# Optimization experiments

Hardware: AMD Instinct MI355X
Metric: run time of the kernel (lower is better)

## Reference

```python
import jax, jax.numpy as jnp
import numpy as np

B, S, H = 2, 4096, 1024  # batch, seq_len, hidden_size (= all_head_size)


def setup_inputs() -> dict:
    key = jax.random.key(0)
    ks = jax.random.split(key, 7)
    sc = 1.0 / np.sqrt(H)
    return {
        "hidden_states": jax.random.normal(ks[0], (B, S, H), dtype=jnp.float32),
        "Wq": jax.random.normal(ks[1], (H, H), dtype=jnp.float32) * sc,
        "bq": jnp.zeros((H,), dtype=jnp.float32),
        "Wk": jax.random.normal(ks[2], (H, H), dtype=jnp.float32) * sc,
        "bk": jnp.zeros((H,), dtype=jnp.float32),
        "Wv": jax.random.normal(ks[3], (H, H), dtype=jnp.float32) * sc,
        "bv": jnp.zeros((H,), dtype=jnp.float32),
    }


def reference(hidden_states, Wq, bq, Wk, bk, Wv, bv):
    # QKV projections (weights stored as [in, out] = W.T of torch Linear)
    q = hidden_states @ Wq + bq  # [B,S,H]
    k = hidden_states @ Wk + bk
    v = hidden_states @ Wv + bv
    # Raw attention: no head split, no 1/sqrt(d) scaling (faithful to source)
    scores = jnp.einsum("bqh,bkh->bqk", q, k)  # [B,S,S]
    probs = jax.nn.softmax(scores, axis=-1)
    context = jnp.einsum("bqk,bkh->bqh", probs, v)  # [B,S,H]
    return context
```

## Files before the change

kernel.cpp:

```cpp
#include <hip/hip_runtime.h>
#include <stdint.h>

typedef __attribute__((ext_vector_type(8))) short short8;
typedef __attribute__((ext_vector_type(8))) _Float16 half8;
typedef __attribute__((ext_vector_type(4))) float f32x4;

__device__ __forceinline__ unsigned short f2h(float x) {
  _Float16 h = (_Float16)x;
  return __builtin_bit_cast(unsigned short, h);
}
__device__ __forceinline__ float h2f(unsigned short u) {
  return (float)__builtin_bit_cast(_Float16, u);
}

#define GLOAD16(gsrc, ldst)                                              \
  __builtin_amdgcn_global_load_lds(                                      \
      (const __attribute__((address_space(1))) void*)(gsrc),             \
      (__attribute__((address_space(3))) void*)(ldst), 16, 0, 0)

#define VM(N) asm volatile("s_waitcnt vmcnt(" #N ")" ::: "memory")
#define BARSYNC __builtin_amdgcn_s_barrier()

__global__ __launch_bounds__(256) void split_pair_f16_kernel(
    const float* __restrict__ in, unsigned short* __restrict__ h,
    unsigned short* __restrict__ l) {
  size_t i = (size_t)blockIdx.x * 256 + threadIdx.x;
  float4 v = ((const float4*)in)[i];
  unsigned short h0 = f2h(v.x), h1 = f2h(v.y), h2 = f2h(v.z), h3 = f2h(v.w);
  ((ushort4*)h)[i] = make_ushort4(h0, h1, h2, h3);
  ((ushort4*)l)[i] = make_ushort4(f2h(v.x - h2f(h0)), f2h(v.y - h2f(h1)),
                                  f2h(v.z - h2f(h2)), f2h(v.w - h2f(h3)));
}

__global__ __launch_bounds__(256) void transpose_f16_kernel(
    const float* __restrict__ W, unsigned short* __restrict__ hT,
    int Kd, int Nd) {
  __shared__ float tile[32][33];
  int r = threadIdx.x >> 3;
  int c = (threadIdx.x & 7) * 4;
  int k0 = blockIdx.y * 32, n0 = blockIdx.x * 32;
  float4 v = *(const float4*)&W[(size_t)(k0 + r) * Nd + n0 + c];
  tile[r][c] = v.x; tile[r][c + 1] = v.y; tile[r][c + 2] = v.z; tile[r][c + 3] = v.w;
  __syncthreads();
  size_t o = (size_t)(n0 + r) * Kd + k0 + c;
  *(ushort4*)&hT[o] = make_ushort4(f2h(tile[c + 0][r]), f2h(tile[c + 1][r]),
                                   f2h(tile[c + 2][r]), f2h(tile[c + 3][r]));
}

template <int OM>
__global__ __launch_bounds__(512, 2) void g2_kernel(
    const unsigned short* __restrict__ Ah, const unsigned short* __restrict__ Al,
    const unsigned short* __restrict__ Bh, const float* __restrict__ bias,
    unsigned short* __restrict__ out0, int K, int lda, int ldb, int ldo) {
  __shared__ __align__(16) char smem[3 * 40 * 1024];

  const int t = threadIdx.x;
  const int wid = t >> 6, lane = t & 63;
  const int waveM = wid >> 2, waveN = wid & 3;
  const int lr0 = lane & 15, lk0 = (lane >> 4) * 8;
  const int m0 = blockIdx.y * 256, n0 = blockIdx.x * 128;

  const unsigned short* slot_src[5];
#pragma unroll
  for (int s = 0; s < 5; ++s) {
    int si = 5 * wid + s;
    const unsigned short* base;
    size_t roff;
    if (si < 16)      { base = Ah; roff = (size_t)(m0 + si * 16 + lr0) * lda; }
    else if (si < 32) { base = Al; roff = (size_t)(m0 + (si - 16) * 16 + lr0) * lda; }
    else              { base = Bh; roff = (size_t)(n0 + (si - 32) * 16 + lr0) * ldb; }
    slot_src[s] = base + roff + lk0;
  }

  const int NTILES = K >> 5;
  f32x4 acc[8][2] = {};

#pragma unroll
  for (int tt = 0; tt < 2; ++tt)
#pragma unroll
    for (int s = 0; s < 5; ++s)
      GLOAD16(slot_src[s] + (size_t)tt * 32,
              smem + tt * 40960 + (5 * wid + s) * 1024);
  VM(5);
  BARSYNC;
  __builtin_amdgcn_sched_barrier(0);

  for (int tile = 0; tile < NTILES; ++tile) {
    const int cur = tile % 3;
    const int nxt = (tile + 2) % 3;
    const bool do_stage = (tile + 2) < NTILES;
    const char* cb = smem + cur * 40960;
    char* nb = smem + nxt * 40960;
    half8 bf[2];
#pragma unroll
    for (int p = 0; p < 4; ++p) {
      half8 ahf[2], alf[2];
#pragma unroll
      for (int i = 0; i < 2; ++i) {
        int mg = waveM * 8 + 2 * p + i;
        ahf[i] = *(const half8*)(cb + mg * 1024 + lane * 16);
        alf[i] = *(const half8*)(cb + (16 + mg) * 1024 + lane * 16);
      }
      if (p == 0) {
#pragma unroll
        for (int j = 0; j < 2; ++j) {
          int ng = waveN * 2 + j;
          bf[j] = *(const half8*)(cb + (32 + ng) * 1024 + lane * 16);
        }
      }
      if (do_stage) {
        if (p == 0) {
          GLOAD16(slot_src[0] + (size_t)(tile + 2) * 32, nb + (5 * wid + 0) * 1024);
          GLOAD16(slot_src[1] + (size_t)(tile + 2) * 32, nb + (5 * wid + 1) * 1024);
        } else {
          const int slot = p + 1;
          GLOAD16(slot_src[slot] + (size_t)(tile + 2) * 32,
                  nb + (5 * wid + slot) * 1024);
        }
      }
      __builtin_amdgcn_s_setprio(1);
#pragma unroll
      for (int i = 0; i < 2; ++i)
#pragma unroll
        for (int j = 0; j < 2; ++j) {
          f32x4 c = acc[2 * p + i][j];
          c = __builtin_amdgcn_mfma_f32_16x16x32_f16(ahf[i], bf[j], c, 0, 0, 0);
          c = __builtin_amdgcn_mfma_f32_16x16x32_f16(alf[i], bf[j], c, 0, 0, 0);
          acc[2 * p + i][j] = c;
        }
      __builtin_amdgcn_s_setprio(0);
      if (p < 3) __builtin_amdgcn_s_barrier();
    }
    if (tile + 1 < NTILES) {
      if (do_stage) VM(5); else VM(0);
      BARSYNC;
      __builtin_amdgcn_sched_barrier(0);
    }
  }

  const int or0 = (lane >> 4) * 4;
#pragma unroll
  for (int mm = 0; mm < 8; ++mm)
#pragma unroll
    for (int j = 0; j < 2; ++j)
#pragma unroll
      for (int r = 0; r < 4; ++r) {
        int row = m0 + waveM * 128 + mm * 16 + or0 + r;
        int col = n0 + waveN * 32 + j * 16 + lr0;
        float x = acc[mm][j][r] + bias[col];
        if constexpr (OM == 4) {
          out0[(size_t)row * ldo + col] = f2h(x);
        } else {
          out0[(size_t)col * ldo + row] = f2h(x);
        }
      }
}

__global__ __launch_bounds__(512, 2) void g1_kernel(
    const unsigned short* __restrict__ Abase, size_t Astr, int lda,
    const unsigned short* __restrict__ Bbase, size_t Bstr, int ldb,
    float* __restrict__ outF, size_t Ostr, int ldo, int K) {
  __shared__ __align__(16) char smem[3 * 48 * 1024];
  const int t = threadIdx.x, wid = t >> 6, lane = t & 63;
  const int waveM = wid >> 2, waveN = wid & 3;
  const int lr0 = lane & 15, lk0 = (lane >> 4) * 8;
  const int m0 = blockIdx.y * 256, n0 = blockIdx.x * 128;
  const unsigned short* A = Abase + (size_t)blockIdx.z * Astr;
  const unsigned short* B = Bbase + (size_t)blockIdx.z * Bstr;
  float* out = outF + (size_t)blockIdx.z * Ostr;

  const unsigned short* slot_src[6];
#pragma unroll
  for (int s = 0; s < 6; ++s) {
    int si = 6 * wid + s;
    const unsigned short* p;
    if (si < 16)      p = A + (size_t)(m0 + si * 16 + lr0) * lda + lk0;
    else if (si < 32) p = A + (size_t)(m0 + (si - 16) * 16 + lr0) * lda + 32 + lk0;
    else if (si < 40) p = B + (size_t)(n0 + (si - 32) * 16 + lr0) * ldb + lk0;
    else              p = B + (size_t)(n0 + (si - 40) * 16 + lr0) * ldb + 32 + lk0;
    slot_src[s] = p;
  }

  const int NTILES = K >> 6;
  f32x4 acc[8][2] = {};

#pragma unroll
  for (int tt = 0; tt < 2; ++tt)
#pragma unroll
    for (int s = 0; s < 6; ++s)
      GLOAD16(slot_src[s] + (size_t)tt * 64,
              smem + tt * 49152 + (6 * wid + s) * 1024);
  VM(6);
  BARSYNC;
  __builtin_amdgcn_sched_barrier(0);

  for (int tile = 0; tile < NTILES; ++tile) {
    const int cur = tile % 3, nxt = (tile + 2) % 3;
    const bool do_stage = (tile + 2) < NTILES;
    const char* cb = smem + cur * 49152;
    char* nb = smem + nxt * 49152;
    half8 blo[2], bhi[2];
#pragma unroll
    for (int p = 0; p < 4; ++p) {
      half8 alo[2], ahi[2];
#pragma unroll
      for (int i = 0; i < 2; ++i) {
        int mg = waveM * 8 + 2 * p + i;
        alo[i] = *(const half8*)(cb + mg * 1024 + lane * 16);
        ahi[i] = *(const half8*)(cb + (16 + mg) * 1024 + lane * 16);
      }
      if (p == 0) {
#pragma unroll
        for (int j = 0; j < 2; ++j) {
          int ng = waveN * 2 + j;
          blo[j] = *(const half8*)(cb + (32 + ng) * 1024 + lane * 16);
          bhi[j] = *(const half8*)(cb + (40 + ng) * 1024 + lane * 16);
        }
      }
      if (do_stage && p < 3) {
#pragma unroll
        for (int s = 0; s < 2; ++s) {
          int slot = 2 * p + s;
          GLOAD16(slot_src[slot] + (size_t)(tile + 2) * 64,
                  nb + (6 * wid + slot) * 1024);
        }
      }
      __builtin_amdgcn_s_setprio(1);
#pragma unroll
      for (int i = 0; i < 2; ++i)
#pragma unroll
        for (int j = 0; j < 2; ++j) {
          f32x4 c = acc[2 * p + i][j];
          c = __builtin_amdgcn_mfma_f32_16x16x32_f16(alo[i], blo[j], c, 0, 0, 0);
          c = __builtin_amdgcn_mfma_f32_16x16x32_f16(ahi[i], bhi[j], c, 0, 0, 0);
          acc[2 * p + i][j] = c;
        }
      __builtin_amdgcn_s_setprio(0);
      if (p < 3) __builtin_amdgcn_s_barrier();
    }
    if (tile + 1 < NTILES) {
      if (do_stage) VM(6); else VM(0);
      BARSYNC;
      __builtin_amdgcn_sched_barrier(0);
    }
  }

  const int or0 = (lane >> 4) * 4;
#pragma unroll
  for (int mm = 0; mm < 8; ++mm)
#pragma unroll
    for (int j = 0; j < 2; ++j)
#pragma unroll
      for (int r = 0; r < 4; ++r)
        out[(size_t)(m0 + waveM * 128 + mm * 16 + or0 + r) * ldo +
            (n0 + waveN * 32 + j * 16 + lr0)] = acc[mm][j][r];
}

__global__ __launch_bounds__(256) void softmax_rows_kernel(
    const float* Sm, unsigned short* P, int ncol, int pld) {
  const int t = threadIdx.x;
  const float* srow = Sm + (size_t)blockIdx.x * ncol;
  float4 v[4];
  float m = -3.4e38f;
#pragma unroll
  for (int i = 0; i < 4; ++i) {
    v[i] = ((const float4*)srow)[t + 256 * i];
    m = fmaxf(m, fmaxf(fmaxf(v[i].x, v[i].y), fmaxf(v[i].z, v[i].w)));
  }
#pragma unroll
  for (int off = 32; off >= 1; off >>= 1) m = fmaxf(m, __shfl_down(m, off));
  __shared__ float redm[4];
  if ((t & 63) == 0) redm[t >> 6] = m;
  __syncthreads();
  m = fmaxf(fmaxf(redm[0], redm[1]), fmaxf(redm[2], redm[3]));
  float s = 0.f;
#pragma unroll
  for (int i = 0; i < 4; ++i) {
    v[i].x = __expf(v[i].x - m);
    v[i].y = __expf(v[i].y - m);
    v[i].z = __expf(v[i].z - m);
    v[i].w = __expf(v[i].w - m);
    s += v[i].x + v[i].y + v[i].z + v[i].w;
  }
#pragma unroll
  for (int off = 32; off >= 1; off >>= 1) s += __shfl_down(s, off);
  __shared__ float reds[4];
  if ((t & 63) == 0) reds[t >> 6] = s;
  __syncthreads();
  s = reds[0] + reds[1] + reds[2] + reds[3];
  float inv = 1.f / s;
  unsigned short* prow = P + (size_t)blockIdx.x * pld;
#pragma unroll
  for (int i = 0; i < 4; ++i) {
    ushort4 o = make_ushort4(f2h(v[i].x * inv), f2h(v[i].y * inv),
                             f2h(v[i].z * inv), f2h(v[i].w * inv));
    ((ushort4*)prow)[t + 256 * i] = o;
  }
}

extern "C" void kernel_launch(void* const* d_in, const int* in_sizes, int n_in,
                              void* d_out, int out_size, void* d_ws, size_t ws_size,
                              hipStream_t stream) {
  const float* hs = (const float*)d_in[0];
  const float* Wq = (const float*)d_in[1];
  const float* bq = (const float*)d_in[2];
  const float* Wk = (const float*)d_in[3];
  const float* bk = (const float*)d_in[4];
  const float* Wv = (const float*)d_in[5];
  const float* bv = (const float*)d_in[6];
  float* out = (float*)d_out;

  constexpr int Ss = 4096, Hh = 1024;
  constexpr int Mm = 8192;
  constexpr size_t TOK = (size_t)Ss * Hh;
  char* ws = (char*)d_ws;
  const size_t MB = 1024 * 1024;

  unsigned short* qh = (unsigned short*)(ws + 0 * MB);
  unsigned short* kh = (unsigned short*)(ws + 16 * MB);
  unsigned short* vT = (unsigned short*)(ws + 32 * MB);
  char* rb = ws + 48 * MB;
  unsigned short* hs_h = (unsigned short*)(rb + 0 * MB);
  unsigned short* hs_l = (unsigned short*)(rb + 16 * MB);
  unsigned short* Wqh = (unsigned short*)(rb + 32 * MB);
  unsigned short* Wkh = (unsigned short*)(rb + 34 * MB);
  unsigned short* Wvh = (unsigned short*)(rb + 36 * MB);
  float* Sf = (float*)rb;

  const bool big = ws_size >= (size_t)176 * MB;

  split_pair_f16_kernel<<<dim3(Mm * Hh / 1024), 256, 0, stream>>>(hs, hs_h, hs_l);
  transpose_f16_kernel<<<dim3(32, 32), 256, 0, stream>>>(Wq, Wqh, Hh, Hh);
  transpose_f16_kernel<<<dim3(32, 32), 256, 0, stream>>>(Wk, Wkh, Hh, Hh);
  transpose_f16_kernel<<<dim3(32, 32), 256, 0, stream>>>(Wv, Wvh, Hh, Hh);

  g2_kernel<4><<<dim3(8, 32), 512, 0, stream>>>(hs_h, hs_l, Wqh, bq, qh, Hh, Hh, Hh, Hh);
  g2_kernel<4><<<dim3(8, 32), 512, 0, stream>>>(hs_h, hs_l, Wkh, bk, kh, Hh, Hh, Hh, Hh);
  g2_kernel<2><<<dim3(8, 32), 512, 0, stream>>>(hs_h, hs_l, Wvh, bv, vT, Hh, Hh, Hh, Mm);

  if (big) {
    g1_kernel<<<dim3(32, 16, 2), 512, 0, stream>>>(
        qh, TOK, Hh, kh, TOK, Hh, Sf, (size_t)Ss * Ss, Ss, Hh);
    softmax_rows_kernel<<<dim3(2 * Ss), 256, 0, stream>>>(
        Sf, (unsigned short*)Sf, Ss, 2 * Ss);
    g1_kernel<<<dim3(8, 16, 2), 512, 0, stream>>>(
        (const unsigned short*)Sf, (size_t)Ss * 2 * Ss, 2 * Ss,
        vT, (size_t)Ss, Mm, out, TOK, Hh, Ss);
  } else {
    float* Sb = (float*)rb;
    unsigned short* Pb = (unsigned short*)(rb + 64 * MB);
    for (int b = 0; b < 2; ++b) {
      g1_kernel<<<dim3(32, 16, 1), 512, 0, stream>>>(
          qh + b * TOK, 0, Hh, kh + b * TOK, 0, Hh, Sb, 0, Ss, Hh);
      softmax_rows_kernel<<<dim3(Ss), 256, 0, stream>>>(Sb, Pb, Ss, Ss);
      g1_kernel<<<dim3(8, 16, 1), 512, 0, stream>>>(
          Pb, 0, Ss, vT + (size_t)b * Ss, 0, Mm, out + b * TOK, 0, Hh, Ss);
    }
  }
}
```

Before: 417.3 us.

## Fuse QKV projections into one wide-tile GEMM and widen QK^T tiles

The three separate Q/K/V projection GEMMs become a single kernel over a concatenated transposed weight buffer, using 256x256 output tiles and routing each column slab to the matching output and bias. A new single-precision-operand QK^T kernel also uses 256x256 tiles in place of the previous 256x128 tiles. Both changes aim to cut launches and reuse each A tile across more output columns, which lowers global and LDS traffic per FLOP. The cost is more accumulator registers per thread (8x4 fragments), which may pressure occupancy, plus per-element branching in the QKV epilogue.

```diff
diff --git a/kernel.cpp b/kernel.cpp
--- a/kernel.cpp
+++ b/kernel.cpp
@@ -47,51 +47,49 @@
                                    f2h(tile[c + 2][r]), f2h(tile[c + 3][r]));
 }
 
-template <int OM>
-__global__ __launch_bounds__(512, 2) void g2_kernel(
+__global__ __launch_bounds__(512, 2) void qkv_kernel(
     const unsigned short* __restrict__ Ah, const unsigned short* __restrict__ Al,
-    const unsigned short* __restrict__ Bh, const float* __restrict__ bias,
-    unsigned short* __restrict__ out0, int K, int lda, int ldb, int ldo) {
-  __shared__ __align__(16) char smem[3 * 40 * 1024];
-
-  const int t = threadIdx.x;
-  const int wid = t >> 6, lane = t & 63;
+    const unsigned short* __restrict__ WT, const float* __restrict__ bq,
+    const float* __restrict__ bk, const float* __restrict__ bv,
+    unsigned short* __restrict__ qh, unsigned short* __restrict__ kh,
+    unsigned short* __restrict__ vT) {
+  __shared__ __align__(16) char smem[3 * 48 * 1024];
+  constexpr int lda = 1024, ldb = 1024, K = 1024;
+  const int t = threadIdx.x, wid = t >> 6, lane = t & 63;
   const int waveM = wid >> 2, waveN = wid & 3;
   const int lr0 = lane & 15, lk0 = (lane >> 4) * 8;
-  const int m0 = blockIdx.y * 256, n0 = blockIdx.x * 128;
-
-  const unsigned short* slot_src[5];
-#pragma unroll
-  for (int s = 0; s < 5; ++s) {
-    int si = 5 * wid + s;
-    const unsigned short* base;
-    size_t roff;
-    if (si < 16)      { base = Ah; roff = (size_t)(m0 + si * 16 + lr0) * lda; }
-    else if (si < 32) { base = Al; roff = (size_t)(m0 + (si - 16) * 16 + lr0) * lda; }
-    else              { base = Bh; roff = (size_t)(n0 + (si - 32) * 16 + lr0) * ldb; }
-    slot_src[s] = base + roff + lk0;
+  const int m0 = blockIdx.y * 256, n0 = blockIdx.x * 256;
+
+  const unsigned short* slot_src[6];
+#pragma unroll
+  for (int s = 0; s < 6; ++s) {
+    int si = 6 * wid + s;
+    const unsigned short* p;
+    if (si < 16)      p = Ah + (size_t)(m0 + si * 16 + lr0) * lda + lk0;
+    else if (si < 32) p = Al + (size_t)(m0 + (si - 16) * 16 + lr0) * lda + lk0;
+    else              p = WT + (size_t)(n0 + (si - 32) * 16 + lr0) * ldb + lk0;
+    slot_src[s] = p;
   }
 
   const int NTILES = K >> 5;
-  f32x4 acc[8][2] = {};
+  f32x4 acc[8][4] = {};
 
 #pragma unroll
   for (int tt = 0; tt < 2; ++tt)
 #pragma unroll
-    for (int s = 0; s < 5; ++s)
+    for (int s = 0; s < 6; ++s)
       GLOAD16(slot_src[s] + (size_t)tt * 32,
-              smem + tt * 40960 + (5 * wid + s) * 1024);
-  VM(5);
+              smem + tt * 49152 + (6 * wid + s) * 1024);
+  VM(6);
   BARSYNC;
   __builtin_amdgcn_sched_barrier(0);
 
   for (int tile = 0; tile < NTILES; ++tile) {
-    const int cur = tile % 3;
-    const int nxt = (tile + 2) % 3;
+    const int cur = tile % 3, nxt = (tile + 2) % 3;
     const bool do_stage = (tile + 2) < NTILES;
-    const char* cb = smem + cur * 40960;
-    char* nb = smem + nxt * 40960;
-    half8 bf[2];
+    const char* cb = smem + cur * 49152;
+    char* nb = smem + nxt * 49152;
+    half8 bf[4];
 #pragma unroll
     for (int p = 0; p < 4; ++p) {
       half8 ahf[2], alf[2];
@@ -99,30 +97,28 @@
       for (int i = 0; i < 2; ++i) {
         int mg = waveM * 8 + 2 * p + i;
         ahf[i] = *(const half8*)(cb + mg * 1024 + lane * 16);
-        alf[i] = *(const half8*)(cb + (16 + mg) * 1024 + lane * 16);
+        alf[i] = *(const half8*)(cb + 16384 + mg * 1024 + lane * 16);
       }
       if (p == 0) {
 #pragma unroll
-        for (int j = 0; j < 2; ++j) {
-          int ng = waveN * 2 + j;
-          bf[j] = *(const half8*)(cb + (32 + ng) * 1024 + lane * 16);
-        }
-      }
-      if (do_stage) {
-        if (p == 0) {
-          GLOAD16(slot_src[0] + (size_t)(tile + 2) * 32, nb + (5 * wid + 0) * 1024);
-          GLOAD16(slot_src[1] + (size_t)(tile + 2) * 32, nb + (5 * wid + 1) * 1024);
-        } else {
-          const int slot = p + 1;
+        for (int j = 0; j < 4; ++j) {
+          int ng = waveN * 4 + j;
+          bf[j] = *(const half8*)(cb + 32768 + ng * 1024 + lane * 16);
+        }
+      }
+      if (do_stage && p < 3) {
+#pragma unroll
+        for (int s = 0; s < 2; ++s) {
+          int slot = 2 * p + s;
           GLOAD16(slot_src[slot] + (size_t)(tile + 2) * 32,
-                  nb + (5 * wid + slot) * 1024);
+                  nb + (6 * wid + slot) * 1024);
         }
       }
       __builtin_amdgcn_s_setprio(1);
 #pragma unroll
       for (int i = 0; i < 2; ++i)
 #pragma unroll
-        for (int j = 0; j < 2; ++j) {
+        for (int j = 0; j < 4; ++j) {
           f32x4 c = acc[2 * p + i][j];
           c = __builtin_amdgcn_mfma_f32_16x16x32_f16(ahf[i], bf[j], c, 0, 0, 0);
           c = __builtin_amdgcn_mfma_f32_16x16x32_f16(alf[i], bf[j], c, 0, 0, 0);
@@ -132,28 +128,119 @@
       if (p < 3) __builtin_amdgcn_s_barrier();
     }
     if (tile + 1 < NTILES) {
-      if (do_stage) VM(5); else VM(0);
+      if (do_stage) VM(6); else VM(0);
       BARSYNC;
       __builtin_amdgcn_sched_barrier(0);
     }
   }
 
   const int or0 = (lane >> 4) * 4;
+  const int slab = n0 >> 10;
 #pragma unroll
   for (int mm = 0; mm < 8; ++mm)
 #pragma unroll
-    for (int j = 0; j < 2; ++j)
+    for (int j = 0; j < 4; ++j)
 #pragma unroll
       for (int r = 0; r < 4; ++r) {
         int row = m0 + waveM * 128 + mm * 16 + or0 + r;
-        int col = n0 + waveN * 32 + j * 16 + lr0;
-        float x = acc[mm][j][r] + bias[col];
-        if constexpr (OM == 4) {
-          out0[(size_t)row * ldo + col] = f2h(x);
+        int col = (n0 & 1023) + waveN * 64 + j * 16 + lr0;
+        float x = acc[mm][j][r];
+        if (slab == 0) {
+          qh[(size_t)row * 1024 + col] = f2h(x + bq[col]);
+        } else if (slab == 1) {
+          kh[(size_t)row * 1024 + col] = f2h(x + bk[col]);
         } else {
-          out0[(size_t)col * ldo + row] = f2h(x);
-        }
-      }
+          vT[(size_t)col * 8192 + row] = f2h(x + bv[col]);
+        }
+      }
+}
+
+__global__ __launch_bounds__(512, 2) void g1q_kernel(
+    const unsigned short* __restrict__ Abase, size_t Astr, int lda,
+    const unsigned short* __restrict__ Bbase, size_t Bstr, int ldb,
+    float* __restrict__ outF, size_t Ostr, int ldo, int K) {
+  __shared__ __align__(16) char smem[3 * 32 * 1024];
+  const int t = threadIdx.x, wid = t >> 6, lane = t & 63;
+  const int waveM = wid >> 2, waveN = wid & 3;
+  const int lr0 = lane & 15, lk0 = (lane >> 4) * 8;
+  const int m0 = blockIdx.y * 256, n0 = blockIdx.x * 256;
+  const unsigned short* A = Abase + (size_t)blockIdx.z * Astr;
+  const unsigned short* B = Bbase + (size_t)blockIdx.z * Bstr;
+  float* out = outF + (size_t)blockIdx.z * Ostr;
+
+  const unsigned short* slot_src[4];
+#pragma unroll
+  for (int s = 0; s < 4; ++s) {
+    int si = 4 * wid + s;
+    const unsigned short* p;
+    if (si < 16) p = A + (size_t)(m0 + si * 16 + lr0) * lda + lk0;
+    else         p = B + (size_t)(n0 + (si - 16) * 16 + lr0) * ldb + lk0;
+    slot_src[s] = p;
+  }
+
+  const int NTILES = K >> 5;
+  f32x4 acc[8][4] = {};
+
+#pragma unroll
+  for (int tt = 0; tt < 2; ++tt)
+#pragma unroll
+    for (int s = 0; s < 4; ++s)
+      GLOAD16(slot_src[s] + (size_t)tt * 32,
+              smem + tt * 32768 + (4 * wid + s) * 1024);
+  VM(4);
+  BARSYNC;
+  __builtin_amdgcn_sched_barrier(0);
+
+  for (int tile = 0; tile < NTILES; ++tile) {
+    const int cur = tile % 3, nxt = (tile + 2) % 3;
+    const bool do_stage = (tile + 2) < NTILES;
+    const char* cb = smem + cur * 32768;
+    char* nb = smem + nxt * 32768;
+    half8 bf[4];
+#pragma unroll
+    for (int p = 0; p < 4; ++p) {
+      half8 af[2];
+#pragma unroll
+      for (int i = 0; i < 2; ++i) {
+        int mg = waveM * 8 + 2 * p + i;
+        af[i] = *(const half8*)(cb + mg * 1024 + lane * 16);
+      }
+      if (p == 0) {
+#pragma unroll
+        for (int j = 0; j < 4; ++j) {
+          int ng = waveN * 4 + j;
+          bf[j] = *(const half8*)(cb + 16384 + ng * 1024 + lane * 16);
+        }
+      }
+      if (do_stage)
+        GLOAD16(slot_src[p] + (size_t)(tile + 2) * 32,
+                nb + (4 * wid + p) * 1024);
+      __builtin_amdgcn_s_setprio(1);
+#pragma unroll
+      for (int i = 0; i < 2; ++i)
+#pragma unroll
+        for (int j = 0; j < 4; ++j)
+          acc[2 * p + i][j] = __builtin_amdgcn_mfma_f32_16x16x32_f16(
+              af[i], bf[j], acc[2 * p + i][j], 0, 0, 0);
+      __builtin_amdgcn_s_setprio(0);
+      if (p < 3) __builtin_amdgcn_s_barrier();
+    }
+    if (tile + 1 < NTILES) {
+      if (do_stage) VM(4); else VM(0);
+      BARSYNC;
+      __builtin_amdgcn_sched_barrier(0);
+    }
+  }
+
+  const int or0 = (lane >> 4) * 4;
+#pragma unroll
+  for (int mm = 0; mm < 8; ++mm)
+#pragma unroll
+    for (int j = 0; j < 4; ++j)
+#pragma unroll
+      for (int r = 0; r < 4; ++r)
+        out[(size_t)(m0 + waveM * 128 + mm * 16 + or0 + r) * ldo +
+            (n0 + waveN * 64 + j * 16 + lr0)] = acc[mm][j][r];
 }
 
 __global__ __launch_bounds__(512, 2) void g1_kernel(
@@ -322,24 +409,23 @@
   char* rb = ws + 48 * MB;
   unsigned short* hs_h = (unsigned short*)(rb + 0 * MB);
   unsigned short* hs_l = (unsigned short*)(rb + 16 * MB);
-  unsigned short* Wqh = (unsigned short*)(rb + 32 * MB);
-  unsigned short* Wkh = (unsigned short*)(rb + 34 * MB);
-  unsigned short* Wvh = (unsigned short*)(rb + 36 * MB);
+  unsigned short* WT = (unsigned short*)(rb + 32 * MB);
   float* Sf = (float*)rb;
 
   const bool big = ws_size >= (size_t)176 * MB;
 
   split_pair_f16_kernel<<<dim3(Mm * Hh / 1024), 256, 0, stream>>>(hs, hs_h, hs_l);
-  transpose_f16_kernel<<<dim3(32, 32), 256, 0, stream>>>(Wq, Wqh, Hh, Hh);
-  transpose_f16_kernel<<<dim3(32, 32), 256, 0, stream>>>(Wk, Wkh, Hh, Hh);
-  transpose_f16_kernel<<<dim3(32, 32), 256, 0, stream>>>(Wv, Wvh, Hh, Hh);
-
-  g2_kernel<4><<<dim3(8, 32), 512, 0, stream>>>(hs_h, hs_l, Wqh, bq, qh, Hh, Hh, Hh, Hh);
-  g2_kernel<4><<<dim3(8, 32), 512, 0, stream>>>(hs_h, hs_l, Wkh, bk, kh, Hh, Hh, Hh, Hh);
-  g2_kernel<2><<<dim3(8, 32), 512, 0, stream>>>(hs_h, hs_l, Wvh, bv, vT, Hh, Hh, Hh, Mm);
+  transpose_f16_kernel<<<dim3(32, 32), 256, 0, stream>>>(Wq, WT, Hh, Hh);
+  transpose_f16_kernel<<<dim3(32, 32), 256, 0, stream>>>(
+      Wk, WT + (size_t)1024 * 1024, Hh, Hh);
+  transpose_f16_kernel<<<dim3(32, 32), 256, 0, stream>>>(
+      Wv, WT + (size_t)2048 * 1024, Hh, Hh);
+
+  qkv_kernel<<<dim3(12, 32), 512, 0, stream>>>(
+      hs_h, hs_l, WT, bq, bk, bv, qh, kh, vT);
 
   if (big) {
-    g1_kernel<<<dim3(32, 16, 2), 512, 0, stream>>>(
+    g1q_kernel<<<dim3(16, 16, 2), 512, 0, stream>>>(
         qh, TOK, Hh, kh, TOK, Hh, Sf, (size_t)Ss * Ss, Ss, Hh);
     softmax_rows_kernel<<<dim3(2 * Ss), 256, 0, stream>>>(
         Sf, (unsigned short*)Sf, Ss, 2 * Ss);
@@ -350,7 +436,7 @@
     float* Sb = (float*)rb;
     unsigned short* Pb = (unsigned short*)(rb + 64 * MB);
     for (int b = 0; b < 2; ++b) {
-      g1_kernel<<<dim3(32, 16, 1), 512, 0, stream>>>(
+      g1q_kernel<<<dim3(16, 16, 1), 512, 0, stream>>>(
           qh + b * TOK, 0, Hh, kh + b * TOK, 0, Hh, Sb, 0, Ss, Hh);
       softmax_rows_kernel<<<dim3(Ss), 256, 0, stream>>>(Sb, Pb, Ss, Ss);
       g1_kernel<<<dim3(8, 16, 1), 512, 0, stream>>>(
```

Result: slower. 426.5 us (+2.2%).
